# Kernel optimization log

Measured on AMD Instinct MI355X. Metric: run time of the kernel, lower is better.

The kernel has to match this reference:

```python
import jax, jax.numpy as jnp
import numpy as np

B, N, C = 512, 196, 192
HEADS, AGENT = 6, 49
HW = 14  # window side, n = HW*HW


def setup_inputs() -> dict:
    key = jax.random.key(0)
    ks = jax.random.split(key, 16)
    f32 = jnp.float32
    inp = {
        'x': jax.random.normal(ks[0], (B, N, C), f32),
        'qkv_w': jax.random.normal(ks[1], (3 * C, C), f32) * 0.02,
        'qkv_b': jnp.zeros((3 * C,), f32),
        'proj_w': jax.random.normal(ks[2], (C, C), f32) * 0.02,
        'proj_b': jnp.zeros((C,), f32),
        'dwc_w': jax.random.normal(ks[3], (C, 1, 3, 3), f32) * 0.1,
        'dwc_b': jnp.zeros((C,), f32),
        'an_bias': jax.random.normal(ks[4], (HEADS, AGENT, 7, 7), f32) * 0.02,
        'na_bias': jax.random.normal(ks[5], (HEADS, AGENT, 7, 7), f32) * 0.02,
        'ah_bias': jax.random.normal(ks[6], (1, HEADS, AGENT, HW, 1), f32) * 0.02,
        'aw_bias': jax.random.normal(ks[7], (1, HEADS, AGENT, 1, HW), f32) * 0.02,
        'ha_bias': jax.random.normal(ks[8], (1, HEADS, HW, 1, AGENT), f32) * 0.02,
        'wa_bias': jax.random.normal(ks[9], (1, HEADS, 1, HW, AGENT), f32) * 0.02,
    }
    return inp


def reference(x, qkv_w, qkv_b, proj_w, proj_b, dwc_w, dwc_b,
              an_bias, na_bias, ah_bias, aw_bias, ha_bias, wa_bias):
    b, n, c = x.shape
    heads, agent_num = an_bias.shape[0], an_bias.shape[1]
    hd = c // heads
    h = w = int(round(n ** 0.5))
    ps = int(round(agent_num ** 0.5))
    scale = hd ** -0.5

    qkv = x @ qkv_w.T + qkv_b                      # (b, n, 3c)
    q, k, v = jnp.split(qkv, 3, axis=-1)           # each (b, n, c)

    # agent tokens: adaptive avg-pool q spatially to (ps, ps) -- exact stride-r avg pool
    r = h // ps
    agent = q.reshape(b, ps, r, ps, r, c).mean(axis=(2, 4)).reshape(b, agent_num, c)

    qh = q.reshape(b, n, heads, hd).transpose(0, 2, 1, 3)          # (b,h,n,d)
    kh = k.reshape(b, n, heads, hd).transpose(0, 2, 1, 3)
    vh = v.reshape(b, n, heads, hd).transpose(0, 2, 1, 3)
    ag = agent.reshape(b, agent_num, heads, hd).transpose(0, 2, 1, 3)  # (b,h,a,d)

    # stage 1: agent <- kv attention, with interpolated + separable biases
    pb1 = jax.image.resize(an_bias, (heads, agent_num, h, w), method='bilinear')
    pb1 = pb1.reshape(heads, agent_num, n)
    pb2 = (ah_bias + aw_bias).reshape(heads, agent_num, n)
    agent_attn = jax.nn.softmax(
        scale * jnp.einsum('bhad,bhnd->bhan', ag, kh) + pb1 + pb2, axis=-1)
    agent_v = jnp.einsum('bhan,bhnd->bhad', agent_attn, vh)        # (b,h,a,d)

    # stage 2: query <- agent attention
    ab1 = jax.image.resize(na_bias, (heads, agent_num, h, w), method='bilinear')
    ab1 = ab1.reshape(heads, agent_num, n).transpose(0, 2, 1)      # (h,n,a)
    ab2 = (ha_bias + wa_bias).reshape(heads, n, agent_num)
    q_attn = jax.nn.softmax(
        scale * jnp.einsum('bhnd,bhad->bhna', qh, ag) + ab1 + ab2, axis=-1)
    out = jnp.einsum('bhna,bhad->bhnd', q_attn, agent_v)
    out = out.transpose(0, 2, 1, 3).reshape(b, n, c)

    # depthwise-conv residual on v
    v_img = v.reshape(b, h, w, c).transpose(0, 3, 1, 2)            # NCHW
    dw = jax.lax.conv_general_dilated(
        v_img, dwc_w, (1, 1), ((1, 1), (1, 1)),
        dimension_numbers=('NCHW', 'OIHW', 'NCHW'), feature_group_count=c)
    dw = dw + dwc_b[None, :, None, None]
    out = out + dw.transpose(0, 2, 3, 1).reshape(b, n, c)

    return out @ proj_w.T + proj_b
```

## Files before the change

kernel.cpp:

```cpp
#include <hip/hip_runtime.h>

typedef unsigned short u16;
typedef __bf16 bf16x8 __attribute__((ext_vector_type(8)));
typedef float f32x4 __attribute__((ext_vector_type(4)));

#define SCALE 0.17677669529663687f

__device__ __forceinline__ float bf2f(u16 u) {
  union { unsigned int i; float f; } x; x.i = ((unsigned int)u) << 16; return x.f;
}
__device__ __forceinline__ u16 f2bf(float f) {
  union { float f; unsigned int i; } x; x.f = f;
  unsigned int i = x.i;
  return (u16)((i + 0x7fffu + ((i >> 16) & 1u)) >> 16);
}
__device__ __forceinline__ uint4 pack8(const u16* h) {
  uint4 r;
  r.x = (unsigned)h[0] | ((unsigned)h[1] << 16);
  r.y = (unsigned)h[2] | ((unsigned)h[3] << 16);
  r.z = (unsigned)h[4] | ((unsigned)h[5] << 16);
  r.w = (unsigned)h[6] | ((unsigned)h[7] << 16);
  return r;
}
__device__ __forceinline__ uint2 pk4(float a, float b, float c, float d) {
  uint2 r;
  r.x = (unsigned)f2bf(a) | ((unsigned)f2bf(b) << 16);
  r.y = (unsigned)f2bf(c) | ((unsigned)f2bf(d) << 16);
  return r;
}
__device__ __forceinline__ bf16x8 zfrag() {
  bf16x8 z;
  #pragma unroll
  for (int j = 0; j < 8; ++j) z[j] = (__bf16)0.0f;
  return z;
}
__device__ __forceinline__ uint2 shfl_u2(uint2 v, int src) {
  uint2 r;
  r.x = (unsigned)__shfl((int)v.x, src);
  r.y = (unsigned)__shfl((int)v.y, src);
  return r;
}

#define LSTR 72
#define ASTR 200

__global__ __launch_bounds__(256) void k_qkv(
    const float* __restrict__ Ag, const u16* __restrict__ Wq, const float* __restrict__ biasg,
    u16* __restrict__ qo, u16* __restrict__ ko, u16* __restrict__ vo)
{
  __shared__ __align__(16) u16 As[128 * ASTR];
  __shared__ __align__(16) u16 Bs[64 * ASTR];
  const int mt = blockIdx.x;
  const int tid = threadIdx.x, lane = tid & 63, wid = tid >> 6;
  const int wm = wid >> 1, wn = wid & 1;
  const int lm = lane & 15, kg = lane >> 4;

  #pragma unroll
  for (int i = 0; i < 12; ++i) {
    int c = tid + i * 256;
    int row = c / 24, cc = (c % 24) * 8;
    const float* s = Ag + (size_t)(mt * 128 + row) * 192 + cc;
    float f[8];
    *(float4*)f = *(const float4*)s;
    *(float4*)(f + 4) = *(const float4*)(s + 4);
    u16 h[8];
    #pragma unroll
    for (int j = 0; j < 8; ++j) h[j] = f2bf(f[j]);
    *(uint4*)(As + row * ASTR + cc) = pack8(h);
  }

  const int aoff = (wm * 64 + lm) * ASTR + kg * 8;
  const int boff = (wn * 32 + lm) * ASTR + kg * 8;

  for (int nt = 0; nt < 9; ++nt) {
    __syncthreads();
    #pragma unroll
    for (int i = 0; i < 6; ++i) {
      int c = tid + i * 256;
      int row = c / 24, cc = (c % 24) * 8;
      *(uint4*)(Bs + row * ASTR + cc) =
          *(const uint4*)(Wq + (size_t)(nt * 64 + row) * 192 + cc);
    }
    __syncthreads();

    f32x4 acc[4][2] = {};
    #pragma unroll
    for (int ks = 0; ks < 6; ++ks) {
      bf16x8 bfr[2];
      #pragma unroll
      for (int nf = 0; nf < 2; ++nf)
        bfr[nf] = *(const bf16x8*)(Bs + boff + nf * 16 * ASTR + ks * 32);
      #pragma unroll
      for (int mf = 0; mf < 4; ++mf) {
        bf16x8 afr = *(const bf16x8*)(As + aoff + mf * 16 * ASTR + ks * 32);
        #pragma unroll
        for (int nf = 0; nf < 2; ++nf)
          acc[mf][nf] = __builtin_amdgcn_mfma_f32_16x16x32_bf16(afr, bfr[nf], acc[mf][nf], 0, 0, 0);
      }
    }

    #pragma unroll
    for (int mf = 0; mf < 4; ++mf) {
      int m0 = mt * 128 + wm * 64 + mf * 16 + kg * 4;
      #pragma unroll
      for (int nf = 0; nf < 2; ++nf) {
        int col = nt * 64 + wn * 32 + nf * 16 + lm;
        float bias = biasg[col];
        int which = col / 192, cc = col - which * 192;
        int hh = cc >> 5, dd = cc & 31;
        u16* dst = (which == 0) ? qo : (which == 1) ? ko : vo;
        #pragma unroll
        for (int r = 0; r < 4; ++r) {
          int m = m0 + r;
          int bq = m / 196, tok = m - bq * 196;
          dst[(((size_t)bq * 6 + hh) * 196 + tok) * 32 + dd] = f2bf(acc[mf][nf][r] + bias);
        }
      }
    }
  }
}

__global__ __launch_bounds__(256) void k_proj(
    const u16* __restrict__ Ag, const float* __restrict__ Wg, const float* __restrict__ biasg,
    float* __restrict__ og)
{
  __shared__ __align__(16) u16 As[128 * LSTR];
  __shared__ __align__(16) u16 Bh[64 * LSTR];
  __shared__ __align__(16) u16 Bl[64 * LSTR];
  const int mt = blockIdx.x / 3, nt = blockIdx.x % 3;
  const int tid = threadIdx.x, lane = tid & 63, wid = tid >> 6;
  const int wm = wid >> 1, wn = wid & 1;
  const int lm = lane & 15, kg = lane >> 4;

  f32x4 acc[4][2] = {};
  const int aoffbase = (wm * 64 + lm) * LSTR + kg * 8;
  const int boffbase = (wn * 32 + lm) * LSTR + kg * 8;

  for (int kt = 0; kt < 3; ++kt) {
    #pragma unroll
    for (int i = 0; i < 4; ++i) {
      int c = tid + i * 256;
      int row = c >> 3, cc = (c & 7) * 8;
      *(uint4*)(As + row * LSTR + cc) =
          *(const uint4*)(Ag + (size_t)(mt * 128 + row) * 192 + kt * 64 + cc);
    }
    #pragma unroll
    for (int i = 0; i < 2; ++i) {
      int c = tid + i * 256;
      int row = c >> 3, cc = (c & 7) * 8;
      const float* s = Wg + (size_t)(nt * 64 + row) * 192 + kt * 64 + cc;
      float f[8];
      *(float4*)f = *(const float4*)s;
      *(float4*)(f + 4) = *(const float4*)(s + 4);
      u16 h[8], l[8];
      #pragma unroll
      for (int j = 0; j < 8; ++j) {
        h[j] = f2bf(f[j]);
        l[j] = f2bf(f[j] - bf2f(h[j]));
      }
      *(uint4*)(Bh + row * LSTR + cc) = pack8(h);
      *(uint4*)(Bl + row * LSTR + cc) = pack8(l);
    }
    __syncthreads();
    #pragma unroll
    for (int ks = 0; ks < 2; ++ks) {
      bf16x8 bh_[2], bl_[2];
      #pragma unroll
      for (int nf = 0; nf < 2; ++nf) {
        bh_[nf] = *(const bf16x8*)(Bh + boffbase + nf * 16 * LSTR + ks * 32);
        bl_[nf] = *(const bf16x8*)(Bl + boffbase + nf * 16 * LSTR + ks * 32);
      }
      #pragma unroll
      for (int mf = 0; mf < 4; ++mf) {
        bf16x8 af = *(const bf16x8*)(As + aoffbase + mf * 16 * LSTR + ks * 32);
        #pragma unroll
        for (int nf = 0; nf < 2; ++nf) {
          acc[mf][nf] = __builtin_amdgcn_mfma_f32_16x16x32_bf16(af, bh_[nf], acc[mf][nf], 0, 0, 0);
          acc[mf][nf] = __builtin_amdgcn_mfma_f32_16x16x32_bf16(af, bl_[nf], acc[mf][nf], 0, 0, 0);
        }
      }
    }
    __syncthreads();
  }

  #pragma unroll
  for (int mf = 0; mf < 4; ++mf) {
    int m0 = mt * 128 + wm * 64 + mf * 16 + kg * 4;
    #pragma unroll
    for (int nf = 0; nf < 2; ++nf) {
      int col = nt * 64 + wn * 32 + nf * 16 + lm;
      float bias = biasg[col];
      #pragma unroll
      for (int r = 0; r < 4; ++r)
        og[(size_t)(m0 + r) * 192 + col] = acc[mf][nf][r] + bias;
    }
  }
}

__global__ __launch_bounds__(256) void k_pool(const u16* __restrict__ qg, u16* __restrict__ agg)
{
  int idx = blockIdx.x * 256 + threadIdx.x;
  int d8 = idx & 3;
  int a = (idx >> 2) % 49;
  int bh = idx / (49 * 4);
  int py = a / 7, px = a - py * 7;
  int n0 = (py * 2) * 14 + px * 2;
  const u16* qb = qg + (size_t)bh * 196 * 32 + d8 * 8;
  uint4 r0 = *(const uint4*)(qb + n0 * 32);
  uint4 r1 = *(const uint4*)(qb + (n0 + 1) * 32);
  uint4 r2 = *(const uint4*)(qb + (n0 + 14) * 32);
  uint4 r3 = *(const uint4*)(qb + (n0 + 15) * 32);
  const u16 *p0 = (const u16*)&r0, *p1 = (const u16*)&r1, *p2 = (const u16*)&r2, *p3 = (const u16*)&r3;
  u16 o[8];
  #pragma unroll
  for (int j = 0; j < 8; ++j)
    o[j] = f2bf(0.25f * (bf2f(p0[j]) + bf2f(p1[j]) + bf2f(p2[j]) + bf2f(p3[j])));
  *(uint4*)(agg + (size_t)idx * 8) = pack8(o);
}

__device__ __forceinline__ void lerpw(int i, int& j0, int& j1, float& f) {
  float xx = 0.5f * i - 0.25f;
  int j = (int)floorf(xx);
  f = xx - j;
  if (j < 0) { j = 0; f = 0.f; }
  j0 = j;
  j1 = (j + 1 > 6) ? 6 : j + 1;
}
__device__ __forceinline__ float bilin7(const float* src, int y, int x) {
  int y0, y1, x0, x1; float fy, fx;
  lerpw(y, y0, y1, fy); lerpw(x, x0, x1, fx);
  float v00 = src[y0 * 7 + x0], v01 = src[y0 * 7 + x1];
  float v10 = src[y1 * 7 + x0], v11 = src[y1 * 7 + x1];
  return (1.f - fy) * ((1.f - fx) * v00 + fx * v01) + fy * ((1.f - fx) * v10 + fx * v11);
}
__global__ __launch_bounds__(256) void k_bias(
    const float* __restrict__ an_, const float* __restrict__ na_,
    const float* __restrict__ ah_, const float* __restrict__ aw_,
    const float* __restrict__ ha_, const float* __restrict__ wa_,
    const float* __restrict__ qw_,
    float* __restrict__ b1, float* __restrict__ b2, u16* __restrict__ wq)
{
  int i = blockIdx.x * 256 + threadIdx.x;
  const int T1 = 6 * 49 * 208;
  const int T2 = 6 * 196 * 64;
  const int T3 = 576 * 192;
  if (i < T1) {
    int n = i % 208, a = (i / 208) % 49, h = i / (208 * 49);
    float v = 0.f;
    if (n < 196) {
      int y = n / 14, x = n - y * 14;
      v = bilin7(an_ + (h * 49 + a) * 49, y, x)
        + ah_[(h * 49 + a) * 14 + y] + aw_[(h * 49 + a) * 14 + x];
    }
    b1[i] = v;
  } else if (i < T1 + T2) {
    int j = i - T1;
    int a = j & 63, n = (j >> 6) % 196, h = j / (196 * 64);
    float v = 0.f;
    if (a < 49) {
      int y = n / 14, x = n - y * 14;
      v = bilin7(na_ + (h * 49 + a) * 49, y, x)
        + ha_[(h * 14 + y) * 49 + a] + wa_[(h * 14 + x) * 49 + a];
    }
    b2[j] = v;
  } else if (i < T1 + T2 + T3) {
    int j = i - T1 - T2;
    wq[j] = f2bf(qw_[j]);
  }
}

#define PSTR 216
#define QSTR 72
#define VSTR 40

__global__ __launch_bounds__(256, 4) void k_attn(
    const u16* __restrict__ qg, const u16* __restrict__ kgl, const u16* __restrict__ vgl,
    const u16* __restrict__ agg, const float* __restrict__ b1p, const float* __restrict__ b2p,
    const float* __restrict__ dwcw, const float* __restrict__ dwcb,
    u16* __restrict__ preg)
{
  __shared__ __align__(16) u16 vt[32 * PSTR];
  __shared__ __align__(16) u16 vrm[196 * VSTR];
  __shared__ __align__(16) u16 avt[32 * QSTR];
  __shared__ __align__(16) float wdl[320];

  const int bh = blockIdx.x, h = bh % 6, b = bh / 6;
  const int tid = threadIdx.x, lane = tid & 63, w = tid >> 6;
  const int lm = lane & 15, kg = lane >> 4;
  const size_t base = (size_t)bh * (196 * 32);

  for (int c = tid; c < 784; c += 256) {
    int row = c >> 2, d0 = (c & 3) * 8;
    uint4 vv = *(const uint4*)(vgl + base + row * 32 + d0);
    *(uint4*)(vrm + row * VSTR + d0) = vv;
    const u16* pv = (const u16*)&vv;
    #pragma unroll
    for (int j = 0; j < 8; ++j) vt[(d0 + j) * PSTR + row] = pv[j];
  }
  for (int c = tid; c < 192; c += 256) {
    int row = c / 6, col = 98 + c % 6;
    ((unsigned*)vt)[row * (PSTR / 2) + col] = 0;
  }
  for (int c = tid; c < 320; c += 256) {
    if (c < 288) {
      int tap = c >> 5, d = c & 31;
      wdl[tap * 32 + d] = dwcw[h * 288 + d * 9 + tap];
    } else {
      wdl[c] = dwcb[h * 32 + (c - 288)];
    }
  }

  const size_t agbase = (size_t)bh * 49 * 32;
  bf16x8 agw;
  {
    int a = 16 * w + lm;
    agw = (a < 49) ? *(const bf16x8*)(agg + agbase + a * 32 + kg * 8) : zfrag();
  }

  f32x4 acc1[13];
  #pragma unroll
  for (int t = 0; t < 13; ++t) {
    bf16x8 afr = *(const bf16x8*)(kgl + base + (16 * t + lm) * 32 + kg * 8);
    acc1[t] = __builtin_amdgcn_mfma_f32_16x16x32_bf16(afr, agw, (f32x4){0.f, 0.f, 0.f, 0.f}, 0, 0, 0);
  }

  const int arow = 16 * w + lm;
  uint2 p1pk[13];
  {
    const float* b1base = b1p + ((size_t)(h * 49 + arow) * 208 + 4 * kg);
    #pragma unroll
    for (int t = 0; t < 13; ++t) {
      f32x4 bv = (arow < 49) ? *(const f32x4*)(b1base + 16 * t) : (f32x4){0.f, 0.f, 0.f, 0.f};
      #pragma unroll
      for (int r = 0; r < 4; ++r) acc1[t][r] = acc1[t][r] * SCALE + bv[r];
    }
    float mx = -1e30f;
    #pragma unroll
    for (int t = 0; t < 12; ++t)
      #pragma unroll
      for (int r = 0; r < 4; ++r) mx = fmaxf(mx, acc1[t][r]);
    if (kg == 0) {
      #pragma unroll
      for (int r = 0; r < 4; ++r) mx = fmaxf(mx, acc1[12][r]);
    }
    mx = fmaxf(mx, __shfl_xor(mx, 16));
    mx = fmaxf(mx, __shfl_xor(mx, 32));
    float sum = 0.f;
    #pragma unroll
    for (int t = 0; t < 13; ++t) {
      #pragma unroll
      for (int r = 0; r < 4; ++r) {
        float e = (t < 12 || kg == 0) ? __expf(acc1[t][r] - mx) : 0.f;
        acc1[t][r] = e; sum += e;
      }
    }
    sum += __shfl_xor(sum, 16);
    sum += __shfl_xor(sum, 32);
    const float inv = 1.0f / sum;
    #pragma unroll
    for (int t = 0; t < 13; ++t)
      p1pk[t] = pk4(acc1[t][0] * inv, acc1[t][1] * inv, acc1[t][2] * inv, acc1[t][3] * inv);
  }

  __syncthreads();

  f32x4 accav[2] = {{0.f, 0.f, 0.f, 0.f}, {0.f, 0.f, 0.f, 0.f}};
  const int sl = (lane & 15) | (((2 * kg) & 3) << 4);
  const int sh = (lane & 15) | (((2 * kg + 1) & 3) << 4);
  #pragma unroll
  for (int kt = 0; kt < 6; ++kt) {
    uint2 e0 = shfl_u2(p1pk[2 * kt], sl);
    uint2 e1 = shfl_u2(p1pk[2 * kt + 1], sl);
    uint2 o0 = shfl_u2(p1pk[2 * kt], sh);
    uint2 o1 = shfl_u2(p1pk[2 * kt + 1], sh);
    uint2 lo = (kg & 2) ? e1 : e0;
    uint2 hi = (kg & 2) ? o1 : o0;
    union { uint4 u; bf16x8 v; } a_;
    a_.u = make_uint4(lo.x, lo.y, hi.x, hi.y);
    #pragma unroll
    for (int nt = 0; nt < 2; ++nt) {
      bf16x8 bfr = *(const bf16x8*)(vt + (16 * nt + lm) * PSTR + kt * 32 + kg * 8);
      accav[nt] = __builtin_amdgcn_mfma_f32_16x16x32_bf16(a_.v, bfr, accav[nt], 0, 0, 0);
    }
  }
  {
    union { uint4 u; bf16x8 v; } a_;
    a_.u = make_uint4(p1pk[12].x, p1pk[12].y, 0u, 0u);
    #pragma unroll
    for (int nt = 0; nt < 2; ++nt) {
      uint2 vv = *(const uint2*)(vt + (16 * nt + lm) * PSTR + 192 + kg * 4);
      union { uint4 u; bf16x8 v; } b_;
      b_.u = make_uint4(vv.x, vv.y, 0u, 0u);
      accav[nt] = __builtin_amdgcn_mfma_f32_16x16x32_bf16(a_.v, b_.v, accav[nt], 0, 0, 0);
    }
  }

  #pragma unroll
  for (int nt = 0; nt < 2; ++nt)
    *(uint2*)(avt + (16 * nt + lm) * QSTR + 16 * w + 4 * kg) =
        pk4(accav[nt][0], accav[nt][1], accav[nt][2], accav[nt][3]);

  bf16x8 qf[4];
  #pragma unroll
  for (int i = 0; i < 4; ++i) {
    int nt = w + 4 * i;
    int row = 16 * nt + lm;
    if (nt < 13 && row < 196)
      qf[i] = *(const bf16x8*)(qg + base + row * 32 + kg * 8);
    else
      qf[i] = zfrag();
  }
  bf16x8 agf[4];
  #pragma unroll
  for (int mt = 0; mt < 4; ++mt) {
    int a = 16 * mt + lm;
    if (a < 49) agf[mt] = *(const bf16x8*)(agg + agbase + a * 32 + kg * 8);
    else agf[mt] = zfrag();
  }

  __syncthreads();

  #pragma unroll
  for (int i = 0; i < 4; ++i) {
    int nt = w + 4 * i;
    if (nt < 13) {
      const int ncol = 16 * nt + lm;
      f32x4 acc2[4];
      #pragma unroll
      for (int mt = 0; mt < 4; ++mt)
        acc2[mt] = __builtin_amdgcn_mfma_f32_16x16x32_bf16(agf[mt], qf[i], (f32x4){0.f, 0.f, 0.f, 0.f}, 0, 0, 0);
      const float* b2base = b2p + ((size_t)(h * 196 + (ncol < 196 ? ncol : 0)) * 64 + 4 * kg);
      #pragma unroll
      for (int mt = 0; mt < 4; ++mt) {
        f32x4 bv = (ncol < 196) ? *(const f32x4*)(b2base + 16 * mt) : (f32x4){0.f, 0.f, 0.f, 0.f};
        #pragma unroll
        for (int r = 0; r < 4; ++r) acc2[mt][r] = acc2[mt][r] * SCALE + bv[r];
      }
      float mx = -1e30f;
      #pragma unroll
      for (int mt = 0; mt < 3; ++mt)
        #pragma unroll
        for (int r = 0; r < 4; ++r) mx = fmaxf(mx, acc2[mt][r]);
      if (kg == 0) mx = fmaxf(mx, acc2[3][0]);
      mx = fmaxf(mx, __shfl_xor(mx, 16));
      mx = fmaxf(mx, __shfl_xor(mx, 32));
      float sum = 0.f;
      #pragma unroll
      for (int mt = 0; mt < 4; ++mt) {
        #pragma unroll
        for (int r = 0; r < 4; ++r) {
          bool valid = (mt < 3) || (kg == 0 && r == 0);
          float e = valid ? __expf(acc2[mt][r] - mx) : 0.f;
          acc2[mt][r] = e; sum += e;
        }
      }
      sum += __shfl_xor(sum, 16);
      sum += __shfl_xor(sum, 32);
      const float inv = 1.0f / sum;
      uint2 p2pk[4];
      #pragma unroll
      for (int mt = 0; mt < 4; ++mt)
        p2pk[mt] = pk4(acc2[mt][0] * inv, acc2[mt][1] * inv, acc2[mt][2] * inv, acc2[mt][3] * inv);

      f32x4 acc4[2] = {{0.f, 0.f, 0.f, 0.f}, {0.f, 0.f, 0.f, 0.f}};
      #pragma unroll
      for (int kt = 0; kt < 2; ++kt) {
        uint2 e0 = shfl_u2(p2pk[2 * kt], sl);
        uint2 e1 = shfl_u2(p2pk[2 * kt + 1], sl);
        uint2 o0 = shfl_u2(p2pk[2 * kt], sh);
        uint2 o1 = shfl_u2(p2pk[2 * kt + 1], sh);
        uint2 lo = (kg & 2) ? e1 : e0;
        uint2 hi = (kg & 2) ? o1 : o0;
        union { uint4 u; bf16x8 v; } b_;
        b_.u = make_uint4(lo.x, lo.y, hi.x, hi.y);
        #pragma unroll
        for (int mt2 = 0; mt2 < 2; ++mt2) {
          bf16x8 afr = *(const bf16x8*)(avt + (16 * mt2 + lm) * QSTR + kt * 32 + kg * 8);
          acc4[mt2] = __builtin_amdgcn_mfma_f32_16x16x32_bf16(afr, b_.v, acc4[mt2], 0, 0, 0);
        }
      }
      if (ncol < 196) {
        const int y = ncol / 14, x = ncol - y * 14;
        float dw[2][4];
        #pragma unroll
        for (int mt = 0; mt < 2; ++mt) {
          f32x4 bv = *(const f32x4*)(wdl + 288 + 16 * mt + 4 * kg);
          #pragma unroll
          for (int r = 0; r < 4; ++r) dw[mt][r] = bv[r];
        }
        #pragma unroll
        for (int ky = 0; ky < 3; ++ky) {
          int yy = y + ky - 1;
          if (yy < 0 || yy > 13) continue;
          #pragma unroll
          for (int kx = 0; kx < 3; ++kx) {
            int xx = x + kx - 1;
            if (xx < 0 || xx > 13) continue;
            int nv = yy * 14 + xx;
            int tap = ky * 3 + kx;
            #pragma unroll
            for (int mt = 0; mt < 2; ++mt) {
              f32x4 wv = *(const f32x4*)(wdl + tap * 32 + 16 * mt + 4 * kg);
              uint2 vv = *(const uint2*)(vrm + nv * VSTR + 16 * mt + 4 * kg);
              const u16* pv = (const u16*)&vv;
              #pragma unroll
              for (int r = 0; r < 4; ++r)
                dw[mt][r] += wv[r] * bf2f(pv[r]);
            }
          }
        }
        u16* orow = preg + ((size_t)b * 196 + ncol) * 192 + h * 32;
        #pragma unroll
        for (int mt = 0; mt < 2; ++mt)
          *(uint2*)(orow + 16 * mt + 4 * kg) =
              pk4(acc4[mt][0] + dw[mt][0], acc4[mt][1] + dw[mt][1],
                  acc4[mt][2] + dw[mt][2], acc4[mt][3] + dw[mt][3]);
      }
    }
  }
}

extern "C" void kernel_launch(void* const* d_in, const int* in_sizes, int n_in,
                              void* d_out, int out_size, void* d_ws, size_t ws_size,
                              hipStream_t stream)
{
  (void)in_sizes; (void)n_in; (void)out_size;
  const float* x      = (const float*)d_in[0];
  const float* qkv_w  = (const float*)d_in[1];
  const float* qkv_b  = (const float*)d_in[2];
  const float* proj_w = (const float*)d_in[3];
  const float* proj_b = (const float*)d_in[4];
  const float* dwc_w  = (const float*)d_in[5];
  const float* dwc_b  = (const float*)d_in[6];
  const float* an_b   = (const float*)d_in[7];
  const float* na_b   = (const float*)d_in[8];
  const float* ah_b   = (const float*)d_in[9];
  const float* aw_b   = (const float*)d_in[10];
  const float* ha_b   = (const float*)d_in[11];
  const float* wa_b   = (const float*)d_in[12];

  const size_t SZ_QKV = (size_t)512 * 6 * 196 * 32 * 2;
  const size_t SZ_AG  = (size_t)512 * 6 * 49 * 32 * 2;
  const size_t SZ_B1  = (((size_t)6 * 49 * 208 * 4) + 255) & ~(size_t)255;
  const size_t SZ_B2  = (size_t)6 * 196 * 64 * 4;
  const size_t SZ_WQ  = (((size_t)576 * 192 * 2) + 255) & ~(size_t)255;

  char* ws = (char*)d_ws;
  u16*   qb    = (u16*)(ws);
  u16*   kb    = (u16*)(ws + SZ_QKV);
  u16*   vb    = (u16*)(ws + 2 * SZ_QKV);
  u16*   agb   = (u16*)(ws + 3 * SZ_QKV);
  float* b1    = (float*)(ws + 3 * SZ_QKV + SZ_AG);
  float* b2    = (float*)(ws + 3 * SZ_QKV + SZ_AG + SZ_B1);
  u16*   preb  = (u16*)(ws + 3 * SZ_QKV + SZ_AG + SZ_B1 + SZ_B2);
  u16*   wqb   = (u16*)(ws + 3 * SZ_QKV + SZ_AG + SZ_B1 + SZ_B2 + SZ_QKV);

  const size_t need = 3 * SZ_QKV + SZ_AG + SZ_B1 + SZ_B2 + SZ_QKV + SZ_WQ;
  if (ws_size < need) return;

  const int TOT = 6 * 49 * 208 + 6 * 196 * 64 + 576 * 192;
  k_bias<<<(TOT + 255) / 256, 256, 0, stream>>>(an_b, na_b, ah_b, aw_b, ha_b, wa_b, qkv_w, b1, b2, wqb);
  k_qkv<<<784, 256, 0, stream>>>(x, wqb, qkv_b, qb, kb, vb);
  k_pool<<<2352, 256, 0, stream>>>(qb, agb);
  k_attn<<<3072, 256, 0, stream>>>(qb, kb, vb, agb, b1, b2, dwc_w, dwc_b, preb);
  k_proj<<<784 * 3, 256, 0, stream>>>(preb, proj_w, proj_b, (float*)d_out);
}
```

Baseline: 192.5 us.

## Split QKV GEMM into smaller tiles per output group and transpose MFMA operands

The QKV projection kernel now uses 64-row token tiles and one of q/k/v per block, giving 4704 blocks instead of 784 for more parallelism. The MFMA operands are swapped so each lane holds four consecutive channels, which allows packed 8-byte bf16 stores and a vectorized bias load in place of scalar 2-byte scattered stores. The cost is that each x tile is loaded and converted from fp32 three times, and there is less reuse per block.

After: 189.0 us. No clear change (-1.8%).

```diff
diff --git a/kernel.cpp b/kernel.cpp
--- a/kernel.cpp
+++ b/kernel.cpp
@@ -48,18 +48,18 @@
     const float* __restrict__ Ag, const u16* __restrict__ Wq, const float* __restrict__ biasg,
     u16* __restrict__ qo, u16* __restrict__ ko, u16* __restrict__ vo)
 {
-  __shared__ __align__(16) u16 As[128 * ASTR];
+  __shared__ __align__(16) u16 As[64 * ASTR];
   __shared__ __align__(16) u16 Bs[64 * ASTR];
-  const int mt = blockIdx.x;
+  const int og = blockIdx.x / 1568, mt = blockIdx.x % 1568;
   const int tid = threadIdx.x, lane = tid & 63, wid = tid >> 6;
-  const int wm = wid >> 1, wn = wid & 1;
+  const int wt = wid >> 1, wc = wid & 1;
   const int lm = lane & 15, kg = lane >> 4;
 
   #pragma unroll
-  for (int i = 0; i < 12; ++i) {
+  for (int i = 0; i < 6; ++i) {
     int c = tid + i * 256;
     int row = c / 24, cc = (c % 24) * 8;
-    const float* s = Ag + (size_t)(mt * 128 + row) * 192 + cc;
+    const float* s = Ag + (size_t)(mt * 64 + row) * 192 + cc;
     float f[8];
     *(float4*)f = *(const float4*)s;
     *(float4*)(f + 4) = *(const float4*)(s + 4);
@@ -69,52 +69,47 @@
     *(uint4*)(As + row * ASTR + cc) = pack8(h);
   }
 
-  const int aoff = (wm * 64 + lm) * ASTR + kg * 8;
-  const int boff = (wn * 32 + lm) * ASTR + kg * 8;
-
-  for (int nt = 0; nt < 9; ++nt) {
+  u16* const dst = (og == 0) ? qo : (og == 1) ? ko : vo;
+
+  for (int nt = 0; nt < 3; ++nt) {
     __syncthreads();
     #pragma unroll
     for (int i = 0; i < 6; ++i) {
       int c = tid + i * 256;
       int row = c / 24, cc = (c % 24) * 8;
       *(uint4*)(Bs + row * ASTR + cc) =
-          *(const uint4*)(Wq + (size_t)(nt * 64 + row) * 192 + cc);
+          *(const uint4*)(Wq + (size_t)(og * 192 + nt * 64 + row) * 192 + cc);
     }
     __syncthreads();
 
-    f32x4 acc[4][2] = {};
+    f32x4 acc[2][2] = {};
     #pragma unroll
     for (int ks = 0; ks < 6; ++ks) {
-      bf16x8 bfr[2];
-      #pragma unroll
-      for (int nf = 0; nf < 2; ++nf)
-        bfr[nf] = *(const bf16x8*)(Bs + boff + nf * 16 * ASTR + ks * 32);
-      #pragma unroll
-      for (int mf = 0; mf < 4; ++mf) {
-        bf16x8 afr = *(const bf16x8*)(As + aoff + mf * 16 * ASTR + ks * 32);
-        #pragma unroll
-        for (int nf = 0; nf < 2; ++nf)
-          acc[mf][nf] = __builtin_amdgcn_mfma_f32_16x16x32_bf16(afr, bfr[nf], acc[mf][nf], 0, 0, 0);
-      }
-    }
-
-    #pragma unroll
-    for (int mf = 0; mf < 4; ++mf) {
-      int m0 = mt * 128 + wm * 64 + mf * 16 + kg * 4;
-      #pragma unroll
-      for (int nf = 0; nf < 2; ++nf) {
-        int col = nt * 64 + wn * 32 + nf * 16 + lm;
-        float bias = biasg[col];
-        int which = col / 192, cc = col - which * 192;
-        int hh = cc >> 5, dd = cc & 31;
-        u16* dst = (which == 0) ? qo : (which == 1) ? ko : vo;
-        #pragma unroll
-        for (int r = 0; r < 4; ++r) {
-          int m = m0 + r;
-          int bq = m / 196, tok = m - bq * 196;
-          dst[(((size_t)bq * 6 + hh) * 196 + tok) * 32 + dd] = f2bf(acc[mf][nf][r] + bias);
-        }
+      bf16x8 xfr[2];
+      #pragma unroll
+      for (int tf = 0; tf < 2; ++tf)
+        xfr[tf] = *(const bf16x8*)(As + (wt * 32 + tf * 16 + lm) * ASTR + ks * 32 + kg * 8);
+      #pragma unroll
+      for (int cf = 0; cf < 2; ++cf) {
+        bf16x8 wfr = *(const bf16x8*)(Bs + (wc * 32 + cf * 16 + lm) * ASTR + ks * 32 + kg * 8);
+        #pragma unroll
+        for (int tf = 0; tf < 2; ++tf)
+          acc[cf][tf] = __builtin_amdgcn_mfma_f32_16x16x32_bf16(wfr, xfr[tf], acc[cf][tf], 0, 0, 0);
+      }
+    }
+
+    #pragma unroll
+    for (int cf = 0; cf < 2; ++cf) {
+      int cc = nt * 64 + wc * 32 + cf * 16 + kg * 4;
+      int hh = cc >> 5, dd = cc & 31;
+      f32x4 bv = *(const f32x4*)(biasg + og * 192 + cc);
+      #pragma unroll
+      for (int tf = 0; tf < 2; ++tf) {
+        int tg = mt * 64 + wt * 32 + tf * 16 + lm;
+        int bq = tg / 196, tok = tg - bq * 196;
+        *(uint2*)(dst + (((size_t)bq * 6 + hh) * 196 + tok) * 32 + dd) =
+            pk4(acc[cf][tf][0] + bv[0], acc[cf][tf][1] + bv[1],
+                acc[cf][tf][2] + bv[2], acc[cf][tf][3] + bv[3]);
       }
     }
   }
@@ -560,7 +555,7 @@
 
   const int TOT = 6 * 49 * 208 + 6 * 196 * 64 + 576 * 192;
   k_bias<<<(TOT + 255) / 256, 256, 0, stream>>>(an_b, na_b, ah_b, aw_b, ha_b, wa_b, qkv_w, b1, b2, wqb);
-  k_qkv<<<784, 256, 0, stream>>>(x, wqb, qkv_b, qb, kb, vb);
+  k_qkv<<<1568 * 3, 256, 0, stream>>>(x, wqb, qkv_b, qb, kb, vb);
   k_pool<<<2352, 256, 0, stream>>>(qb, agb);
   k_attn<<<3072, 256, 0, stream>>>(qb, kb, vb, agb, b1, b2, dwc_w, dwc_b, preb);
   k_proj<<<784 * 3, 256, 0, stream>>>(preb, proj_w, proj_b, (float*)d_out);
```
